# Performance work log

Hardware: AMD Instinct MI355X
Metric: run time of the kernel (lower is better)

The kernel has to match this reference:

```python
import jax, jax.numpy as jnp
import numpy as np

N, NFEAT, NHID, NHEADS, NCLASS = 8192, 512, 64, 8, 40
ALPHA = 0.2
NEG = jnp.float32(-9e15)


def _gat_layer(h, W, a, concat):
    # h: [N, Fin], W: [Fin, Fout], a: [2*Fout, 1]
    Fout = W.shape[1]
    Wh = h @ W                      # [N, Fout]
    f1 = Wh @ a[:Fout]              # [N, 1]
    f2 = Wh @ a[Fout:]              # [N, 1]
    e = jax.nn.leaky_relu(f1 + f2.T, negative_slope=ALPHA)  # [N, N]
    # NOTE: source masks on e > 0 (adj is NOT used) - replicate faithfully
    att = jax.nn.softmax(jnp.where(e > 0, e, NEG), axis=1)
    h_prime = att @ Wh              # [N, Fout]
    return jax.nn.elu(h_prime) if concat else h_prime


def setup_inputs() -> dict:
    key = jax.random.key(0)
    ks = jax.random.split(key, 6)
    x = jax.random.normal(ks[0], (N, NFEAT), dtype=jnp.float32)
    adj = jax.random.randint(ks[1], (N, N), 0, 2).astype(jnp.bool_)  # unused by math, kept for fidelity
    s = 0.1
    W_heads = jax.random.normal(ks[2], (NHEADS, NFEAT, NHID), dtype=jnp.float32) * s
    a_heads = jax.random.normal(ks[3], (NHEADS, 2 * NHID, 1), dtype=jnp.float32) * s
    W_out = jax.random.normal(ks[4], (NHID * NHEADS, NCLASS), dtype=jnp.float32) * s
    a_out = jax.random.normal(ks[5], (2 * NCLASS, 1), dtype=jnp.float32) * s
    return {"x": x, "adj": adj, "W_heads": W_heads, "a_heads": a_heads,
            "W_out": W_out, "a_out": a_out}


def reference(x, adj, W_heads, a_heads, W_out, a_out):
    # multi-head GAT layers (concat=True), vmapped over heads
    heads = jax.vmap(lambda W, a: _gat_layer(x, W, a, True))(W_heads, a_heads)  # [H, N, NHID]
    h = jnp.transpose(heads, (1, 0, 2)).reshape(N, NHEADS * NHID)
    # output attention layer (concat=False), then elu + log_softmax
    out = _gat_layer(h, W_out, a_out, False)
    out = jax.nn.elu(out)
    return jax.nn.log_softmax(out, axis=1)
```

## Files before the change

### kernel.cpp

```cpp
#include <hip/hip_runtime.h>
#include <math.h>

#define N_NODES 8192
#define NFEAT 512
#define NHID 64
#define NHEADS 8
#define NCLASS 40
#define NCHUNK 128
#define CHUNK 64
#define NB 4096

using bf16x8 = __attribute__((ext_vector_type(8))) short;
using f32x4 = __attribute__((ext_vector_type(4))) float;

__device__ __forceinline__ ushort f2b(float f) {
  uint u = __builtin_bit_cast(uint, f);
  u += 0x7FFFu + ((u >> 16) & 1u);
  return (ushort)(u >> 16);
}
__device__ __forceinline__ float b2f(ushort h) {
  uint u = (uint)h << 16;
  return __builtin_bit_cast(float, u);
}
__device__ __forceinline__ uint encf(float f) {
  uint u = __builtin_bit_cast(uint, f);
  return u ^ ((u >> 31) ? 0xFFFFFFFFu : 0x80000000u);
}
__device__ __forceinline__ float decf(uint u) {
  u ^= ((u >> 31) ? 0x80000000u : 0xFFFFFFFFu);
  return __builtin_bit_cast(float, u);
}
__device__ __forceinline__ float3 load_rng(const uint* mm, int head) {
  float h = decf(mm[head * 2]);
  float l = decf(~mm[head * 2 + 1]);
  float scale = (float)NB / fmaxf(h - l, 1e-30f);
  return make_float3(l, scale, h);
}
__device__ __forceinline__ int bucket_of(float v, float lo, float scale) {
  float u = fminf(fmaxf((v - lo) * scale, 0.f), (float)(NB - 1));
  return (int)u;
}

__global__ __launch_bounds__(256) void prep_k(const float* __restrict__ x,
                                              const float* __restrict__ W_heads,
                                              ushort* __restrict__ bth,
                                              ushort* __restrict__ btl,
                                              ushort* __restrict__ xh_,
                                              ushort* __restrict__ xl_) {
  int b = blockIdx.x, t = threadIdx.x;
  if (b < 1024) {
    int gid = b * 256 + t;
    int n = gid >> 9, c = gid & 511;
    int h = n >> 6, f = n & 63;
    float w = W_heads[((size_t)h * NFEAT + c) * NHID + f];
    ushort hh = f2b(w);
    bth[gid] = hh;
    btl[gid] = f2b(w - b2f(hh));
  } else {
    int gid2 = (b - 1024) * 256 + t;
    const float* src = x + (size_t)gid2 * 8;
    float4 v0 = *reinterpret_cast<const float4*>(src);
    float4 v1 = *reinterpret_cast<const float4*>(src + 4);
    float vv[8] = {v0.x, v0.y, v0.z, v0.w, v1.x, v1.y, v1.z, v1.w};
    uint uh[4], ul[4];
#pragma unroll
    for (int k = 0; k < 4; ++k) {
      ushort h0 = f2b(vv[2 * k]), h1 = f2b(vv[2 * k + 1]);
      ushort l0 = f2b(vv[2 * k] - b2f(h0)), l1 = f2b(vv[2 * k + 1] - b2f(h1));
      uh[k] = (uint)h0 | ((uint)h1 << 16);
      ul[k] = (uint)l0 | ((uint)l1 << 16);
    }
    *reinterpret_cast<uint4*>(xh_ + (size_t)gid2 * 8) = make_uint4(uh[0], uh[1], uh[2], uh[3]);
    *reinterpret_cast<uint4*>(xl_ + (size_t)gid2 * 8) = make_uint4(ul[0], ul[1], ul[2], ul[3]);
  }
}

__global__ __launch_bounds__(256) void gemm1_k(const ushort* __restrict__ xh,
                                               const ushort* __restrict__ xl,
                                               const ushort* __restrict__ bth,
                                               const ushort* __restrict__ btl,
                                               const float* __restrict__ a_heads,
                                               float* __restrict__ Wh,
                                               float* __restrict__ f1,
                                               float* __restrict__ f2,
                                               float* __restrict__ meanS,
                                               uint* __restrict__ mm1) {
  const int row0 = blockIdx.x * 128, col0 = blockIdx.y * 128;
  const int tid = threadIdx.x;
  const int wave = tid >> 6, lane = tid & 63;
  const int wr = wave >> 1, wc = wave & 1;
  __shared__ ushort Ah[128 * 40], Al[128 * 40], Bh[128 * 40], Bl[128 * 40];
  __shared__ float cs[2][64];
  __shared__ uint lmax[2], lmin[2];
  if (tid < 2) { lmax[tid] = 0u; lmin[tid] = 0u; }
  if (tid < 128) cs[tid >> 6][tid & 63] = 0.f;
  f32x4 acc[4][4] = {};
  const int sr = tid >> 1, sh = (tid & 1) * 16;
  const int fr = lane & 15, quad = lane >> 4;
  for (int k0 = 0; k0 < NFEAT; k0 += 32) {
    {
      size_t aoff = (size_t)(row0 + sr) * NFEAT + k0 + sh;
      *reinterpret_cast<uint4*>(&Ah[sr * 40 + sh])     = *reinterpret_cast<const uint4*>(xh + aoff);
      *reinterpret_cast<uint4*>(&Ah[sr * 40 + sh + 8]) = *reinterpret_cast<const uint4*>(xh + aoff + 8);
      *reinterpret_cast<uint4*>(&Al[sr * 40 + sh])     = *reinterpret_cast<const uint4*>(xl + aoff);
      *reinterpret_cast<uint4*>(&Al[sr * 40 + sh + 8]) = *reinterpret_cast<const uint4*>(xl + aoff + 8);
      size_t boff = (size_t)(col0 + sr) * NFEAT + k0 + sh;
      *reinterpret_cast<uint4*>(&Bh[sr * 40 + sh])     = *reinterpret_cast<const uint4*>(bth + boff);
      *reinterpret_cast<uint4*>(&Bh[sr * 40 + sh + 8]) = *reinterpret_cast<const uint4*>(bth + boff + 8);
      *reinterpret_cast<uint4*>(&Bl[sr * 40 + sh])     = *reinterpret_cast<const uint4*>(btl + boff);
      *reinterpret_cast<uint4*>(&Bl[sr * 40 + sh + 8]) = *reinterpret_cast<const uint4*>(btl + boff + 8);
    }
    __syncthreads();
    bf16x8 afh[4], afl[4], bfh[4], bfl[4];
#pragma unroll
    for (int q = 0; q < 4; ++q) {
      afh[q] = *reinterpret_cast<const bf16x8*>(&Ah[(wr * 64 + q * 16 + fr) * 40 + quad * 8]);
      afl[q] = *reinterpret_cast<const bf16x8*>(&Al[(wr * 64 + q * 16 + fr) * 40 + quad * 8]);
      bfh[q] = *reinterpret_cast<const bf16x8*>(&Bh[(wc * 64 + q * 16 + fr) * 40 + quad * 8]);
      bfl[q] = *reinterpret_cast<const bf16x8*>(&Bl[(wc * 64 + q * 16 + fr) * 40 + quad * 8]);
    }
#pragma unroll
    for (int qr = 0; qr < 4; ++qr)
#pragma unroll
      for (int qc = 0; qc < 4; ++qc) {
        acc[qr][qc] = __builtin_amdgcn_mfma_f32_16x16x32_bf16(afl[qr], bfh[qc], acc[qr][qc], 0, 0, 0);
        acc[qr][qc] = __builtin_amdgcn_mfma_f32_16x16x32_bf16(afh[qr], bfl[qc], acc[qr][qc], 0, 0, 0);
        acc[qr][qc] = __builtin_amdgcn_mfma_f32_16x16x32_bf16(afh[qr], bfh[qc], acc[qr][qc], 0, 0, 0);
      }
    __syncthreads();
  }
  const int head = blockIdx.y * 2 + wc;
#pragma unroll
  for (int qr = 0; qr < 4; ++qr)
#pragma unroll
    for (int qc = 0; qc < 4; ++qc)
#pragma unroll
      for (int i = 0; i < 4; ++i) {
        int row = row0 + wr * 64 + qr * 16 + quad * 4 + i;
        int col = col0 + wc * 64 + qc * 16 + fr;
        Wh[(size_t)row * NFEAT + col] = acc[qr][qc][i];
      }
  const float* ah = a_heads + head * 2 * NHID;
  float a1v[4], a2v[4];
#pragma unroll
  for (int qc = 0; qc < 4; ++qc) { a1v[qc] = ah[qc * 16 + fr]; a2v[qc] = ah[NHID + qc * 16 + fr]; }
#pragma unroll
  for (int qr = 0; qr < 4; ++qr)
#pragma unroll
    for (int i = 0; i < 4; ++i) {
      float s1 = 0.f, s2 = 0.f;
#pragma unroll
      for (int qc = 0; qc < 4; ++qc) { s1 += acc[qr][qc][i] * a1v[qc]; s2 += acc[qr][qc][i] * a2v[qc]; }
#pragma unroll
      for (int m = 1; m < 16; m <<= 1) { s1 += __shfl_xor(s1, m, 64); s2 += __shfl_xor(s2, m, 64); }
      if (fr == 0) {
        int row = row0 + wr * 64 + qr * 16 + quad * 4 + i;
        f1[(head << 13) + row] = s1;
        f2[(head << 13) + row] = s2;
        atomicMax(&lmax[wc], encf(s2));
        atomicMax(&lmin[wc], ~encf(s2));
      }
    }
#pragma unroll
  for (int qc = 0; qc < 4; ++qc) {
    float v = 0.f;
#pragma unroll
    for (int qr = 0; qr < 4; ++qr)
#pragma unroll
      for (int i = 0; i < 4; ++i) v += acc[qr][qc][i];
    v += __shfl_xor(v, 16, 64);
    v += __shfl_xor(v, 32, 64);
    if (quad == 0) atomicAdd(&cs[wc][qc * 16 + fr], v);
  }
  __syncthreads();
  if (tid < 128) atomicAdd(&meanS[(blockIdx.y * 2 + (tid >> 6)) * NHID + (tid & 63)], cs[tid >> 6][tid & 63]);
  if (tid < 2) {
    atomicMax(&mm1[(blockIdx.y * 2 + tid) * 2], lmax[tid]);
    atomicMax(&mm1[(blockIdx.y * 2 + tid) * 2 + 1], lmin[tid]);
  }
}

__global__ __launch_bounds__(256) void gemm2_k(const float* __restrict__ H,
                                               const float* __restrict__ Wout,
                                               const float* __restrict__ a_out,
                                               float* __restrict__ Wh2,
                                               float* __restrict__ f1b,
                                               float* __restrict__ f2b,
                                               float* __restrict__ meanS2,
                                               uint* __restrict__ mm2) {
  const int row0 = blockIdx.x * 32;
  const int tid = threadIdx.x;
  __shared__ float As[32][33];
  __shared__ float Bs[32][40];
  __shared__ float cs[NCLASS];
  __shared__ uint lmax, lmin;
  if (tid < NCLASS) cs[tid] = 0.f;
  if (tid == 0) { lmax = 0u; lmin = 0u; }
  const int m = tid >> 3;
  const int n0 = (tid & 7) * 5;
  float acc[5] = {};
  for (int k0 = 0; k0 < NFEAT; k0 += 32) {
    {
      int kk = tid & 31, mq = tid >> 5;
#pragma unroll
      for (int r = 0; r < 4; ++r)
        As[kk][mq * 4 + r] = H[(size_t)(row0 + mq * 4 + r) * NFEAT + k0 + kk];
    }
    {
#pragma unroll
      for (int r = 0; r < 5; ++r) {
        int idx = tid + r * 256;
        if (idx < 1280) {
          int c = idx / 40, n = idx - c * 40;
          Bs[c][n] = Wout[(size_t)(k0 + c) * NCLASS + n];
        }
      }
    }
    __syncthreads();
#pragma unroll
    for (int kk = 0; kk < 32; ++kk) {
      float a = As[kk][m];
#pragma unroll
      for (int q = 0; q < 5; ++q) acc[q] += a * Bs[kk][n0 + q];
    }
    __syncthreads();
  }
#pragma unroll
  for (int q = 0; q < 5; ++q) Wh2[(size_t)(row0 + m) * NCLASS + n0 + q] = acc[q];
  float p1 = 0.f, p2 = 0.f;
#pragma unroll
  for (int q = 0; q < 5; ++q) {
    p1 += acc[q] * a_out[n0 + q];
    p2 += acc[q] * a_out[NCLASS + n0 + q];
  }
  p1 += __shfl_xor(p1, 1, 64); p1 += __shfl_xor(p1, 2, 64); p1 += __shfl_xor(p1, 4, 64);
  p2 += __shfl_xor(p2, 1, 64); p2 += __shfl_xor(p2, 2, 64); p2 += __shfl_xor(p2, 4, 64);
  if ((tid & 7) == 0) {
    f1b[row0 + m] = p1;
    f2b[row0 + m] = p2;
    atomicMax(&lmax, encf(p2));
    atomicMax(&lmin, ~encf(p2));
  }
#pragma unroll
  for (int q = 0; q < 5; ++q) atomicAdd(&cs[n0 + q], acc[q]);
  __syncthreads();
  if (tid < NCLASS) atomicAdd(&meanS2[tid], cs[tid]);
  if (tid == 0) { atomicMax(&mm2[0], lmax); atomicMax(&mm2[1], lmin); }
}

__global__ __launch_bounds__(256) void hist_k(const float* __restrict__ f2, const uint* __restrict__ mm,
                                              int* __restrict__ hist) {
  int gid = blockIdx.x * 256 + threadIdx.x;
  int head = gid >> 13;
  float3 rg = load_rng(mm, head);
  atomicAdd(&hist[head * NB + bucket_of(f2[gid], rg.x, rg.y)], 1);
}

__global__ __launch_bounds__(1024) void prefix_k(const int* __restrict__ hist, int* __restrict__ bs) {
  __shared__ int sb[NB];
  int head = blockIdx.x, tid = threadIdx.x;
#pragma unroll
  for (int r = 0; r < NB / 1024; ++r) sb[tid + r * 1024] = hist[head * NB + tid + r * 1024];
  __syncthreads();
  for (int st = 1; st < NB; st <<= 1) {
    int v[NB / 1024];
#pragma unroll
    for (int r = 0; r < NB / 1024; ++r) { int i = tid + r * 1024; v[r] = (i >= st) ? sb[i - st] : 0; }
    __syncthreads();
#pragma unroll
    for (int r = 0; r < NB / 1024; ++r) sb[tid + r * 1024] += v[r];
    __syncthreads();
  }
#pragma unroll
  for (int r = 0; r < NB / 1024; ++r) {
    int b = tid + r * 1024;
    bs[head * (NB + 1) + b] = b ? sb[b - 1] : 0;
  }
  if (tid == 0) bs[head * (NB + 1) + NB] = sb[NB - 1];
}

__global__ __launch_bounds__(256) void scat_k(const float* __restrict__ f2, const uint* __restrict__ mm,
                                              const int* __restrict__ bs, int* __restrict__ cnt,
                                              int* __restrict__ idxs, float* __restrict__ f2s,
                                              float* __restrict__ g) {
  int gid = blockIdx.x * 256 + threadIdx.x;
  int head = gid >> 13, i = gid & 8191;
  float v = f2[gid];
  float3 rg = load_rng(mm, head);
  int b = bucket_of(v, rg.x, rg.y);
  int pos = bs[head * (NB + 1) + b] + atomicAdd(&cnt[head * NB + b], 1);
  int base = head << 13;
  idxs[base + pos] = i;
  f2s[base + pos] = v;
  g[base + pos] = expf(v - rg.z);
}

template <int F, int LD, int COLSTEP>
__global__ __launch_bounds__(64) void scanA_k(const float* __restrict__ Wh,
                                              const float* __restrict__ g,
                                              const int* __restrict__ idxs,
                                              float* __restrict__ S,
                                              float* __restrict__ D,
                                              float* __restrict__ T_,
                                              float* __restrict__ Td) {
  int head = blockIdx.y, chunk = blockIdx.x;
  int lane = threadIdx.x;
  int base = head << 13;
  int kbase = base + chunk * CHUNK;
  int myj = idxs[kbase + lane];
  float myg = g[kbase + lane];
  float acc = 0.f, accD = 0.f;
#pragma unroll
  for (int kk = CHUNK - 1; kk >= 0; --kk) {
    int j = __shfl(myj, kk, 64);
    float gk = __shfl(myg, kk, 64);
    float w = (lane < F) ? Wh[(size_t)j * LD + head * COLSTEP + lane] : 0.f;
    acc += gk * w;
    accD += gk;
    if (lane < F) S[(size_t)(kbase + kk) * F + lane] = acc;
    if (lane == 0) D[kbase + kk] = accD;
  }
  if (lane < F) T_[(size_t)(head * NCHUNK + chunk) * F + lane] = acc;
  if (lane == 0) Td[head * NCHUNK + chunk] = accD;
}

template <int F>
__global__ __launch_bounds__(1024) void scanB_k(float* __restrict__ T_, float* __restrict__ Td) {
  __shared__ float s[NCHUNK * F];
  __shared__ float td[NCHUNK];
  int head = blockIdx.x;
  int tid = threadIdx.x, slot = tid >> 6, lane = tid & 63;
#pragma unroll
  for (int r = 0; r < 8; ++r) {
    int c = r * 16 + slot;
    if (lane < F) s[c * F + lane] = T_[(size_t)(head * NCHUNK + c) * F + lane];
  }
  if (tid < NCHUNK) td[tid] = Td[head * NCHUNK + tid];
  __syncthreads();
  for (int st = 1; st < NCHUNK; st <<= 1) {
    float v[8];
    float tv = 0.f;
#pragma unroll
    for (int r = 0; r < 8; ++r) {
      int c = r * 16 + slot;
      v[r] = (lane < F && c + st < NCHUNK) ? s[(c + st) * F + lane] : 0.f;
    }
    if (tid < NCHUNK && tid + st < NCHUNK) tv = td[tid + st];
    __syncthreads();
#pragma unroll
    for (int r = 0; r < 8; ++r) {
      int c = r * 16 + slot;
      if (lane < F) s[c * F + lane] += v[r];
    }
    if (tid < NCHUNK) td[tid] += tv;
    __syncthreads();
  }
#pragma unroll
  for (int r = 0; r < 8; ++r) {
    int c = r * 16 + slot;
    if (lane < F) T_[(size_t)(head * NCHUNK + c) * F + lane] = s[c * F + lane];
  }
  if (tid < NCHUNK) Td[head * NCHUNK + tid] = td[tid];
}

__global__ __launch_bounds__(256) void query1_k(const float* __restrict__ f1,
                                                const float* __restrict__ f2s,
                                                const int* __restrict__ idxs,
                                                const float* __restrict__ Wh,
                                                const float* __restrict__ S,
                                                const float* __restrict__ D,
                                                const float* __restrict__ T_,
                                                const float* __restrict__ Td,
                                                const uint* __restrict__ mm,
                                                const int* __restrict__ bs,
                                                const float* __restrict__ meanS,
                                                float* __restrict__ H) {
  int w = blockIdx.x * 4 + (threadIdx.x >> 6);
  int lane = threadIdx.x & 63;
  int head = w & 7, i = w >> 3, base = head << 13;
  float t = f1[base + i];
  float3 rg = load_rng(mm, head);
  int B0 = bucket_of(-t, rg.x, rg.y);
  int p0 = bs[head * (NB + 1) + B0], p1 = bs[head * (NB + 1) + B0 + 1];
  float num = 0.f, den = 0.f;
  int cnt = N_NODES - p1;
  if (p1 < N_NODES) {
    int c = p1 >> 6;
    num = S[(size_t)(base + p1) * NHID + lane] +
          ((c + 1 < NCHUNK) ? T_[(size_t)(head * NCHUNK + c + 1) * NHID + lane] : 0.f);
    den = D[base + p1] + ((c + 1 < NCHUNK) ? Td[head * NCHUNK + c + 1] : 0.f);
  }
  for (int p = p0; p < p1; ++p) {
    float v = f2s[base + p];
    if (t + v > 0.f) {
      int j = idxs[base + p];
      float gk = expf(v - rg.z);
      num += gk * Wh[(size_t)j * NFEAT + head * NHID + lane];
      den += gk;
      ++cnt;
    }
  }
  float val = cnt ? num / den : meanS[head * NHID + lane] * (1.f / N_NODES);
  H[(size_t)i * NFEAT + head * NHID + lane] = (val > 0.f) ? val : expm1f(val);
}

__global__ __launch_bounds__(256) void final_k(const float* __restrict__ f1b,
                                               const float* __restrict__ f2bs,
                                               const int* __restrict__ idx2,
                                               const float* __restrict__ Wh2,
                                               const float* __restrict__ S2,
                                               const float* __restrict__ D2,
                                               const float* __restrict__ T2,
                                               const float* __restrict__ Td2,
                                               const uint* __restrict__ mm2,
                                               const int* __restrict__ bs2,
                                               const float* __restrict__ meanS2,
                                               float* __restrict__ out) {
  int i = blockIdx.x * 4 + (threadIdx.x >> 6);
  int lane = threadIdx.x & 63;
  float t = f1b[i];
  float3 rg = load_rng(mm2, 0);
  int B0 = bucket_of(-t, rg.x, rg.y);
  int p0 = bs2[B0], p1 = bs2[B0 + 1];
  float num = 0.f, den = 0.f;
  int cnt = N_NODES - p1;
  if (p1 < N_NODES) {
    int c = p1 >> 6;
    num = (lane < NCLASS) ? (S2[(size_t)p1 * NCLASS + lane] +
                             ((c + 1 < NCHUNK) ? T2[(size_t)(c + 1) * NCLASS + lane] : 0.f))
                          : 0.f;
    den = D2[p1] + ((c + 1 < NCHUNK) ? Td2[c + 1] : 0.f);
  }
  for (int p = p0; p < p1; ++p) {
    float v = f2bs[p];
    if (t + v > 0.f) {
      int j = idx2[p];
      float gk = expf(v - rg.z);
      if (lane < NCLASS) num += gk * Wh2[(size_t)j * NCLASS + lane];
      den += gk;
      ++cnt;
    }
  }
  float o;
  if (lane < NCLASS) {
    float val = cnt ? num / den : meanS2[lane] * (1.f / N_NODES);
    o = (val > 0.f) ? val : expm1f(val);
  } else {
    o = -INFINITY;
  }
  float m = o;
#pragma unroll
  for (int msk = 32; msk; msk >>= 1) m = fmaxf(m, __shfl_xor(m, msk, 64));
  float e = (lane < NCLASS) ? expf(o - m) : 0.f;
#pragma unroll
  for (int msk = 32; msk; msk >>= 1) e += __shfl_xor(e, msk, 64);
  if (lane < NCLASS) out[(size_t)i * NCLASS + lane] = o - m - logf(e);
}

extern "C" void kernel_launch(void* const* d_in, const int* in_sizes, int n_in,
                              void* d_out, int out_size, void* d_ws, size_t ws_size,
                              hipStream_t stream) {
  const float* x       = (const float*)d_in[0];
  const float* W_heads = (const float*)d_in[2];
  const float* a_heads = (const float*)d_in[3];
  const float* W_out   = (const float*)d_in[4];
  const float* a_out   = (const float*)d_in[5];
  float* out = (float*)d_out;

  float* ws = (float*)d_ws;
  size_t o = 0;
  auto alloc = [&](size_t n) { float* p = ws + o; o += (n + 3) & ~(size_t)3; return p; };
  float*  S1     = alloc((size_t)NHEADS * N_NODES * NHID);
  ushort* xh     = (ushort*)S1;
  ushort* xl     = (ushort*)(S1 + (size_t)N_NODES * NFEAT / 2);
  ushort* BTh    = (ushort*)alloc((size_t)NFEAT * NFEAT / 2);
  ushort* BTl    = (ushort*)alloc((size_t)NFEAT * NFEAT / 2);
  float*  Wh     = alloc((size_t)N_NODES * NFEAT);
  float*  H      = alloc((size_t)N_NODES * NFEAT);
  float*  f1     = alloc(NHEADS * N_NODES);
  float*  f2     = alloc(NHEADS * N_NODES);
  float*  f2s    = alloc(NHEADS * N_NODES);
  int*    idxs   = (int*)alloc(NHEADS * N_NODES);
  float*  g1     = alloc(NHEADS * N_NODES);
  float*  D1     = alloc(NHEADS * N_NODES);
  float*  T1     = alloc(NHEADS * NCHUNK * NHID);
  float*  Td1    = alloc(NHEADS * NCHUNK);
  int*    bst1   = (int*)alloc(NHEADS * (NB + 1));
  float*  Wh2    = alloc((size_t)N_NODES * NCLASS);
  float*  S2     = alloc((size_t)N_NODES * NCLASS);
  float*  f1b    = alloc(N_NODES);
  float*  f2b    = alloc(N_NODES);
  float*  f2bs   = alloc(N_NODES);
  int*    idx2   = (int*)alloc(N_NODES);
  float*  g2     = alloc(N_NODES);
  float*  D2     = alloc(N_NODES);
  float*  T2     = alloc(NCHUNK * NCLASS);
  float*  Td2    = alloc(NCHUNK);
  int*    bst2   = (int*)alloc(NB + 1);
  float*  zbase  = ws + o;
  int*    hist1  = (int*)alloc((size_t)NHEADS * NB);
  int*    cnt1   = (int*)alloc((size_t)NHEADS * NB);
  int*    hist2  = (int*)alloc(NB);
  int*    cnt2   = (int*)alloc(NB);
  uint*   mm1    = (uint*)alloc(16);
  uint*   mm2    = (uint*)alloc(4);
  float*  meanS1 = alloc(NHEADS * NHID);
  float*  meanS2 = alloc(64);
  size_t zbytes = (size_t)((ws + o) - zbase) * sizeof(float);
  hipMemsetAsync(zbase, 0, zbytes, stream);

  prep_k<<<1024 + 2048, 256, 0, stream>>>(x, W_heads, BTh, BTl, xh, xl);
  gemm1_k<<<dim3(64, 4), 256, 0, stream>>>(xh, xl, BTh, BTl, a_heads, Wh, f1, f2, meanS1, mm1);
  hist_k<<<(NHEADS * N_NODES) / 256, 256, 0, stream>>>(f2, mm1, hist1);
  prefix_k<<<NHEADS, 1024, 0, stream>>>(hist1, bst1);
  scat_k<<<(NHEADS * N_NODES) / 256, 256, 0, stream>>>(f2, mm1, bst1, cnt1, idxs, f2s, g1);
  scanA_k<NHID, NFEAT, NHID><<<dim3(NCHUNK, NHEADS), 64, 0, stream>>>(Wh, g1, idxs, S1, D1, T1, Td1);
  scanB_k<NHID><<<NHEADS, 1024, 0, stream>>>(T1, Td1);
  query1_k<<<16384, 256, 0, stream>>>(f1, f2s, idxs, Wh, S1, D1, T1, Td1, mm1, bst1, meanS1, H);

  gemm2_k<<<256, 256, 0, stream>>>(H, W_out, a_out, Wh2, f1b, f2b, meanS2, mm2);
  hist_k<<<N_NODES / 256, 256, 0, stream>>>(f2b, mm2, hist2);
  prefix_k<<<1, 1024, 0, stream>>>(hist2, bst2);
  scat_k<<<N_NODES / 256, 256, 0, stream>>>(f2b, mm2, bst2, cnt2, idx2, f2bs, g2);
  scanA_k<NCLASS, NCLASS, 0><<<dim3(NCHUNK, 1), 64, 0, stream>>>(Wh2, g2, idx2, S2, D2, T2, Td2);
  scanB_k<NCLASS><<<1, 1024, 0, stream>>>(T2, Td2);
  final_k<<<2048, 256, 0, stream>>>(f1b, f2bs, idx2, Wh2, S2, D2, T2, Td2, mm2, bst2, meanS2, out);
}
```

Baseline: 561.1 us.

## Fuse x bf16 split into GEMM, fold memset into prep, parallelize chunk scan

The split of x into bf16 hi/lo parts moves from the prep kernel into gemm1's tile loads, so the split arrays are no longer written to and read back from global memory. The workspace memset is replaced by zeroing inside the prep kernel, which removes one launch. scanA now runs 4 waves per chunk, each scanning 16 elements into shared memory before a cross-wave offset combine, which shortens the serial dependency chain from 64 steps to 16. In exchange, x is converted once per column block (4 times) inside gemm1, and scanA uses more shared memory and adds a block barrier.

After: 535.8 us. -4.5%, faster.

```diff
diff --git a/kernel.cpp b/kernel.cpp
--- a/kernel.cpp
+++ b/kernel.cpp
@@ -41,42 +41,22 @@
   return (int)u;
 }
 
-__global__ __launch_bounds__(256) void prep_k(const float* __restrict__ x,
-                                              const float* __restrict__ W_heads,
+__global__ __launch_bounds__(256) void prep_k(const float* __restrict__ W_heads,
                                               ushort* __restrict__ bth,
                                               ushort* __restrict__ btl,
-                                              ushort* __restrict__ xh_,
-                                              ushort* __restrict__ xl_) {
-  int b = blockIdx.x, t = threadIdx.x;
-  if (b < 1024) {
-    int gid = b * 256 + t;
-    int n = gid >> 9, c = gid & 511;
-    int h = n >> 6, f = n & 63;
-    float w = W_heads[((size_t)h * NFEAT + c) * NHID + f];
-    ushort hh = f2b(w);
-    bth[gid] = hh;
-    btl[gid] = f2b(w - b2f(hh));
-  } else {
-    int gid2 = (b - 1024) * 256 + t;
-    const float* src = x + (size_t)gid2 * 8;
-    float4 v0 = *reinterpret_cast<const float4*>(src);
-    float4 v1 = *reinterpret_cast<const float4*>(src + 4);
-    float vv[8] = {v0.x, v0.y, v0.z, v0.w, v1.x, v1.y, v1.z, v1.w};
-    uint uh[4], ul[4];
-#pragma unroll
-    for (int k = 0; k < 4; ++k) {
-      ushort h0 = f2b(vv[2 * k]), h1 = f2b(vv[2 * k + 1]);
-      ushort l0 = f2b(vv[2 * k] - b2f(h0)), l1 = f2b(vv[2 * k + 1] - b2f(h1));
-      uh[k] = (uint)h0 | ((uint)h1 << 16);
-      ul[k] = (uint)l0 | ((uint)l1 << 16);
-    }
-    *reinterpret_cast<uint4*>(xh_ + (size_t)gid2 * 8) = make_uint4(uh[0], uh[1], uh[2], uh[3]);
-    *reinterpret_cast<uint4*>(xl_ + (size_t)gid2 * 8) = make_uint4(ul[0], ul[1], ul[2], ul[3]);
-  }
-}
-
-__global__ __launch_bounds__(256) void gemm1_k(const ushort* __restrict__ xh,
-                                               const ushort* __restrict__ xl,
+                                              float* __restrict__ zbase,
+                                              int zcount) {
+  int gid = blockIdx.x * 256 + threadIdx.x;
+  int n = gid >> 9, c = gid & 511;
+  int h = n >> 6, f = n & 63;
+  float w = W_heads[((size_t)h * NFEAT + c) * NHID + f];
+  ushort hh = f2b(w);
+  bth[gid] = hh;
+  btl[gid] = f2b(w - b2f(hh));
+  if (gid < zcount) zbase[gid] = 0.f;
+}
+
+__global__ __launch_bounds__(256) void gemm1_k(const float* __restrict__ x,
                                                const ushort* __restrict__ bth,
                                                const ushort* __restrict__ btl,
                                                const float* __restrict__ a_heads,
@@ -99,11 +79,24 @@
   const int fr = lane & 15, quad = lane >> 4;
   for (int k0 = 0; k0 < NFEAT; k0 += 32) {
     {
-      size_t aoff = (size_t)(row0 + sr) * NFEAT + k0 + sh;
-      *reinterpret_cast<uint4*>(&Ah[sr * 40 + sh])     = *reinterpret_cast<const uint4*>(xh + aoff);
-      *reinterpret_cast<uint4*>(&Ah[sr * 40 + sh + 8]) = *reinterpret_cast<const uint4*>(xh + aoff + 8);
-      *reinterpret_cast<uint4*>(&Al[sr * 40 + sh])     = *reinterpret_cast<const uint4*>(xl + aoff);
-      *reinterpret_cast<uint4*>(&Al[sr * 40 + sh + 8]) = *reinterpret_cast<const uint4*>(xl + aoff + 8);
+      const float* xs = x + (size_t)(row0 + sr) * NFEAT + k0 + sh;
+      float av[16];
+      *reinterpret_cast<float4*>(&av[0])  = *reinterpret_cast<const float4*>(xs);
+      *reinterpret_cast<float4*>(&av[4])  = *reinterpret_cast<const float4*>(xs + 4);
+      *reinterpret_cast<float4*>(&av[8])  = *reinterpret_cast<const float4*>(xs + 8);
+      *reinterpret_cast<float4*>(&av[12]) = *reinterpret_cast<const float4*>(xs + 12);
+      uint uh[8], ul[8];
+#pragma unroll
+      for (int q = 0; q < 8; ++q) {
+        ushort h0 = f2b(av[2 * q]), h1 = f2b(av[2 * q + 1]);
+        ushort l0 = f2b(av[2 * q] - b2f(h0)), l1 = f2b(av[2 * q + 1] - b2f(h1));
+        uh[q] = (uint)h0 | ((uint)h1 << 16);
+        ul[q] = (uint)l0 | ((uint)l1 << 16);
+      }
+      *reinterpret_cast<uint4*>(&Ah[sr * 40 + sh])     = make_uint4(uh[0], uh[1], uh[2], uh[3]);
+      *reinterpret_cast<uint4*>(&Ah[sr * 40 + sh + 8]) = make_uint4(uh[4], uh[5], uh[6], uh[7]);
+      *reinterpret_cast<uint4*>(&Al[sr * 40 + sh])     = make_uint4(ul[0], ul[1], ul[2], ul[3]);
+      *reinterpret_cast<uint4*>(&Al[sr * 40 + sh + 8]) = make_uint4(ul[4], ul[5], ul[6], ul[7]);
       size_t boff = (size_t)(col0 + sr) * NFEAT + k0 + sh;
       *reinterpret_cast<uint4*>(&Bh[sr * 40 + sh])     = *reinterpret_cast<const uint4*>(bth + boff);
       *reinterpret_cast<uint4*>(&Bh[sr * 40 + sh + 8]) = *reinterpret_cast<const uint4*>(bth + boff + 8);
@@ -296,32 +289,59 @@
 }
 
 template <int F, int LD, int COLSTEP>
-__global__ __launch_bounds__(64) void scanA_k(const float* __restrict__ Wh,
-                                              const float* __restrict__ g,
-                                              const int* __restrict__ idxs,
-                                              float* __restrict__ S,
-                                              float* __restrict__ D,
-                                              float* __restrict__ T_,
-                                              float* __restrict__ Td) {
-  int head = blockIdx.y, chunk = blockIdx.x;
-  int lane = threadIdx.x;
-  int base = head << 13;
-  int kbase = base + chunk * CHUNK;
-  int myj = idxs[kbase + lane];
-  float myg = g[kbase + lane];
+__global__ __launch_bounds__(256) void scanA_k(const float* __restrict__ Wh,
+                                               const float* __restrict__ g,
+                                               const int* __restrict__ idxs,
+                                               float* __restrict__ S,
+                                               float* __restrict__ D,
+                                               float* __restrict__ T_,
+                                               float* __restrict__ Td) {
+  constexpr int PAD = (F == 64) ? 66 : 42;
+  const int head = blockIdx.y, chunk = blockIdx.x;
+  const int tid = threadIdx.x, w = tid >> 6, lane = tid & 63;
+  const int base = head << 13;
+  const int kbase = base + chunk * CHUNK;
+  __shared__ float Sloc[64][PAD];
+  __shared__ float Dloc[64];
+  __shared__ float wtot[4][PAD];
+  __shared__ float wtotD[4];
+  int myj = 0; float myg = 0.f;
+  if (lane < 16) {
+    myj = idxs[kbase + w * 16 + lane];
+    myg = g[kbase + w * 16 + lane];
+  }
   float acc = 0.f, accD = 0.f;
 #pragma unroll
-  for (int kk = CHUNK - 1; kk >= 0; --kk) {
+  for (int kk = 15; kk >= 0; --kk) {
     int j = __shfl(myj, kk, 64);
     float gk = __shfl(myg, kk, 64);
-    float w = (lane < F) ? Wh[(size_t)j * LD + head * COLSTEP + lane] : 0.f;
-    acc += gk * w;
+    float wv = (lane < F) ? Wh[(size_t)j * LD + head * COLSTEP + lane] : 0.f;
+    acc += gk * wv;
     accD += gk;
-    if (lane < F) S[(size_t)(kbase + kk) * F + lane] = acc;
-    if (lane == 0) D[kbase + kk] = accD;
-  }
-  if (lane < F) T_[(size_t)(head * NCHUNK + chunk) * F + lane] = acc;
-  if (lane == 0) Td[head * NCHUNK + chunk] = accD;
+    if (lane < F) Sloc[w * 16 + kk][lane] = acc;
+    if (lane == 0) Dloc[w * 16 + kk] = accD;
+  }
+  if (lane < F) wtot[w][lane] = acc;
+  if (lane == 0) wtotD[w] = accD;
+  __syncthreads();
+  float off = 0.f, offD = 0.f;
+#pragma unroll
+  for (int w2 = 1; w2 < 4; ++w2) {
+    if (w + w2 < 4) {
+      off += (lane < F) ? wtot[w + w2][lane] : 0.f;
+      offD += wtotD[w + w2];
+    }
+  }
+#pragma unroll
+  for (int kk = 0; kk < 16; ++kk) {
+    int e = w * 16 + kk;
+    if (lane < F) S[(size_t)(kbase + e) * F + lane] = Sloc[e][lane] + off;
+    if (lane == 0) D[kbase + e] = Dloc[e] + offD;
+  }
+  if (w == 0) {
+    if (lane < F) T_[(size_t)(head * NCHUNK + chunk) * F + lane] = wtot[0][lane] + off;
+    if (lane == 0) Td[head * NCHUNK + chunk] = wtotD[0] + offD;
+  }
 }
 
 template <int F>
@@ -471,8 +491,6 @@
   size_t o = 0;
   auto alloc = [&](size_t n) { float* p = ws + o; o += (n + 3) & ~(size_t)3; return p; };
   float*  S1     = alloc((size_t)NHEADS * N_NODES * NHID);
-  ushort* xh     = (ushort*)S1;
-  ushort* xl     = (ushort*)(S1 + (size_t)N_NODES * NFEAT / 2);
   ushort* BTh    = (ushort*)alloc((size_t)NFEAT * NFEAT / 2);
   ushort* BTl    = (ushort*)alloc((size_t)NFEAT * NFEAT / 2);
   float*  Wh     = alloc((size_t)N_NODES * NFEAT);
@@ -506,15 +524,14 @@
   uint*   mm2    = (uint*)alloc(4);
   float*  meanS1 = alloc(NHEADS * NHID);
   float*  meanS2 = alloc(64);
-  size_t zbytes = (size_t)((ws + o) - zbase) * sizeof(float);
-  hipMemsetAsync(zbase, 0, zbytes, stream);
-
-  prep_k<<<1024 + 2048, 256, 0, stream>>>(x, W_heads, BTh, BTl, xh, xl);
-  gemm1_k<<<dim3(64, 4), 256, 0, stream>>>(xh, xl, BTh, BTl, a_heads, Wh, f1, f2, meanS1, mm1);
+  int zcount = (int)((ws + o) - zbase);
+
+  prep_k<<<1024, 256, 0, stream>>>(W_heads, BTh, BTl, zbase, zcount);
+  gemm1_k<<<dim3(64, 4), 256, 0, stream>>>(x, BTh, BTl, a_heads, Wh, f1, f2, meanS1, mm1);
   hist_k<<<(NHEADS * N_NODES) / 256, 256, 0, stream>>>(f2, mm1, hist1);
   prefix_k<<<NHEADS, 1024, 0, stream>>>(hist1, bst1);
   scat_k<<<(NHEADS * N_NODES) / 256, 256, 0, stream>>>(f2, mm1, bst1, cnt1, idxs, f2s, g1);
-  scanA_k<NHID, NFEAT, NHID><<<dim3(NCHUNK, NHEADS), 64, 0, stream>>>(Wh, g1, idxs, S1, D1, T1, Td1);
+  scanA_k<NHID, NFEAT, NHID><<<dim3(NCHUNK, NHEADS), 256, 0, stream>>>(Wh, g1, idxs, S1, D1, T1, Td1);
   scanB_k<NHID><<<NHEADS, 1024, 0, stream>>>(T1, Td1);
   query1_k<<<16384, 256, 0, stream>>>(f1, f2s, idxs, Wh, S1, D1, T1, Td1, mm1, bst1, meanS1, H);
 
@@ -522,7 +539,7 @@
   hist_k<<<N_NODES / 256, 256, 0, stream>>>(f2b, mm2, hist2);
   prefix_k<<<1, 1024, 0, stream>>>(hist2, bst2);
   scat_k<<<N_NODES / 256, 256, 0, stream>>>(f2b, mm2, bst2, cnt2, idx2, f2bs, g2);
-  scanA_k<NCLASS, NCLASS, 0><<<dim3(NCHUNK, 1), 64, 0, stream>>>(Wh2, g2, idx2, S2, D2, T2, Td2);
+  scanA_k<NCLASS, NCLASS, 0><<<dim3(NCHUNK, 1), 256, 0, stream>>>(Wh2, g2, idx2, S2, D2, T2, Td2);
   scanB_k<NCLASS><<<1, 1024, 0, stream>>>(T2, Td2);
   final_k<<<2048, 256, 0, stream>>>(f1b, f2bs, idx2, Wh2, S2, D2, T2, Td2, mm2, bst2, meanS2, out);
 }
```
